# Performance work log

Hardware: AMD Instinct MI355X
Metric: run time of the kernel (lower is better)

Reference implementation:

```python
import jax, jax.numpy as jnp
import numpy as np
from jax import lax

B, T, V, E, H, K = 64, 512, 50257, 300, 128, 3


def setup_inputs() -> dict:
    key = jax.random.key(0)
    ks = jax.random.split(key, 16)
    s = 0.05
    return {
        "tokens": jax.random.randint(ks[0], (B, T), 0, V),
        "emb": jax.random.normal(ks[1], (V, E), jnp.float32) * s,
        # forward LSTM (keras gate order i,f,g,o packed along last axis)
        "Wf": jax.random.normal(ks[2], (E, 4 * H), jnp.float32) * s,
        "Uf": jax.random.normal(ks[3], (H, 4 * H), jnp.float32) * s,
        "bf": jnp.zeros((4 * H,), jnp.float32),
        # backward LSTM
        "Wb": jax.random.normal(ks[4], (E, 4 * H), jnp.float32) * s,
        "Ub": jax.random.normal(ks[5], (H, 4 * H), jnp.float32) * s,
        "bb": jnp.zeros((4 * H,), jnp.float32),
        # dense projection to tagset
        "Wd": jax.random.normal(ks[6], (2 * H, K), jnp.float32) * s,
        "bd": jnp.zeros((K,), jnp.float32),
        # tfa.layers.CRF params: inner kernel, chain transitions, boundaries
        "crf_W": jax.random.normal(ks[7], (K, K), jnp.float32) * s,
        "crf_b": jnp.zeros((K,), jnp.float32),
        "chain": jax.random.normal(ks[8], (K, K), jnp.float32) * s,
        "left_b": jax.random.normal(ks[9], (K,), jnp.float32) * s,
        "right_b": jax.random.normal(ks[10], (K,), jnp.float32) * s,
    }


def _lstm(x, W, U, b):
    """Keras LSTM: gates i,f,g,o; sigmoid recurrent act, tanh cell act."""
    xW = jnp.einsum("btd,dh->bth", x, W) + b  # precompute input GEMM [B,T,4H]
    h0 = jnp.zeros((x.shape[0], U.shape[0]), x.dtype)

    def step(carry, xw):
        h, c = carry
        z = xw + h @ U
        i, f, g, o = jnp.split(z, 4, axis=-1)
        c = jax.nn.sigmoid(f) * c + jax.nn.sigmoid(i) * jnp.tanh(g)
        h = jax.nn.sigmoid(o) * jnp.tanh(c)
        return (h, c), h

    _, hs = lax.scan(step, (h0, h0), jnp.swapaxes(xW, 0, 1))  # [T,B,H]
    return jnp.swapaxes(hs, 0, 1)  # [B,T,H]


def _potentials(tokens, emb, Wf, Uf, bf, Wb, Ub, bb, Wd, bd, crf_W, crf_b, left_b, right_b):
    x = emb[tokens]  # [B,T,E]
    h_fwd = _lstm(x, Wf, Uf, bf)
    h_bwd = _lstm(x[:, ::-1], Wb, Ub, bb)[:, ::-1]
    h = jnp.concatenate([h_fwd, h_bwd], axis=-1)  # [B,T,2H]
    logits = h @ Wd + bd                          # [B,T,K]
    pot = logits @ crf_W + crf_b                  # CRF inner kernel
    pot = pot.at[:, 0].add(left_b).at[:, -1].add(right_b)  # boundary energies
    return pot


def _viterbi(pot, trans):
    """Viterbi decode. pot [B,T,K], trans [K,K] (prev->next)."""
    def step(alpha, p):
        scores = alpha[:, :, None] + trans[None]   # [B,K_prev,K_next]
        bp = jnp.argmax(scores, axis=1)            # [B,K]
        alpha = jnp.max(scores, axis=1) + p
        return alpha, bp

    alpha, bps = lax.scan(step, pot[:, 0], jnp.swapaxes(pot[:, 1:], 0, 1))
    last = jnp.argmax(alpha, axis=-1)  # [B]

    def back(tag, bp):
        prev = jnp.take_along_axis(bp, tag[:, None], axis=1)[:, 0]
        return prev, prev

    _, tags = lax.scan(back, last, bps, reverse=True)  # [T-1,B]
    return jnp.concatenate([jnp.swapaxes(tags, 0, 1), last[:, None]], axis=1)


def reference(tokens, emb, Wf, Uf, bf, Wb, Ub, bb, Wd, bd, crf_W, crf_b, chain, left_b, right_b):
    pot = _potentials(tokens, emb, Wf, Uf, bf, Wb, Ub, bb, Wd, bd, crf_W, crf_b, left_b, right_b)
    decoded = _viterbi(pot, chain)  # [B,T] int
    return decoded, pot
```

## Files before the change

### kernel.cpp

```cpp
#include <hip/hip_runtime.h>
#include <hip/hip_bf16.h>
#include <math.h>

#define BATCH 64
#define TSEQ  512
#define BT    (BATCH*TSEQ)
#define EDIM  300
#define HID   128
#define G4    512
#define KTAG  3

typedef __attribute__((ext_vector_type(8))) short bf16x8;
typedef __attribute__((ext_vector_type(8))) unsigned short u16x8;
typedef __attribute__((ext_vector_type(4))) float f32x4;

__device__ __forceinline__ unsigned short bf16rn(float v) {
    unsigned int u = __float_as_uint(v);
    return (unsigned short)((u + 0x7FFF + ((u >> 16) & 1)) >> 16);
}

__global__ __launch_bounds__(256) void split_kernel(
    const int* __restrict__ tokens, const float* __restrict__ emb,
    const float* __restrict__ Wf, const float* __restrict__ Wb,
    unsigned short* __restrict__ Abf, unsigned short* __restrict__ Bbf)
{
    const int gid = blockIdx.x * 256 + threadIdx.x;
    const int NA = BT * 80;
    if (gid < NA) {
        const int m = gid / 80;
        const int q = gid - m * 80;
        const int kp = q * 8;
        const int seg = kp >= 320;
        const int k0 = kp - (seg ? 320 : 0);
        const float* __restrict__ er = emb + (size_t)tokens[m] * EDIM;
        unsigned short o[8];
        #pragma unroll
        for (int i = 0; i < 8; ++i) {
            const int kk = k0 + i;
            const float v = (kk < EDIM) ? er[kk] : 0.f;
            const unsigned short hi = bf16rn(v);
            o[i] = seg ? bf16rn(v - __uint_as_float((unsigned)hi << 16)) : hi;
        }
        u16x8 w = {o[0], o[1], o[2], o[3], o[4], o[5], o[6], o[7]};
        *(u16x8*)(Abf + (size_t)m * 640 + kp) = w;
    } else {
        const int g2 = gid - NA;
        const int c = g2 / 120;
        const int q = g2 - c * 120;
        const int kp = q * 8;
        const int seg = (kp >= 640) ? 2 : (kp >= 320 ? 1 : 0);
        const int k0 = kp - seg * 320;
        const float* __restrict__ W = (c >= 512) ? Wb : Wf;
        const int cc = c & 511;
        unsigned short o[8];
        #pragma unroll
        for (int i = 0; i < 8; ++i) {
            const int kk = k0 + i;
            const float v = (kk < EDIM) ? W[(size_t)kk * G4 + cc] : 0.f;
            const unsigned short hi = bf16rn(v);
            o[i] = (seg == 2) ? bf16rn(v - __uint_as_float((unsigned)hi << 16)) : hi;
        }
        u16x8 w = {o[0], o[1], o[2], o[3], o[4], o[5], o[6], o[7]};
        *(u16x8*)(Bbf + (size_t)c * 960 + kp) = w;
    }
}

#if defined(__has_builtin)
#if __has_builtin(__builtin_amdgcn_global_load_lds)
#define HAVE_GLL 1
#endif
#endif

__device__ __forceinline__ void gll16(const unsigned short* g, unsigned short* lds_base) {
#ifdef HAVE_GLL
    __builtin_amdgcn_global_load_lds(
        (const __attribute__((address_space(1))) unsigned int*)g,
        (__attribute__((address_space(3))) unsigned int*)lds_base, 16, 0, 0);
#else
    const int l = threadIdx.x & 63;
    *(u16x8*)(lds_base + l * 8) = *(const u16x8*)g;
#endif
}

__global__ __launch_bounds__(256) void gemm_bf16(
    const unsigned short* __restrict__ Abf, const unsigned short* __restrict__ Bbf,
    const float* __restrict__ bf, const float* __restrict__ bb,
    float* __restrict__ xW)
{
    const int n0 = blockIdx.x * 128;
    const int m0 = blockIdx.y * 128;
    const int tid = threadIdx.x;
    const int lane = tid & 63;
    const int wv = tid >> 6;

    const int dir = n0 >> 9;
    const float* __restrict__ bias = dir ? bb : bf;
    const int c0 = n0 & 511;

    __shared__ __align__(16) unsigned short As[128 * 32];
    __shared__ __align__(16) unsigned short Bs[128 * 32];

    f32x4 acc[4][4];
    #pragma unroll
    for (int i = 0; i < 4; ++i)
        #pragma unroll
        for (int j = 0; j < 4; ++j)
            acc[i][j] = (f32x4){0.f, 0.f, 0.f, 0.f};

    const int wm = (wv & 1) * 64;
    const int wn = (wv >> 1) * 64;

    const int r0 = 32 * wv + (lane >> 2);
    const unsigned short* Asrc0 = Abf + (size_t)(m0 + r0)      * 640 + (lane & 3) * 8;
    const unsigned short* Asrc1 = Abf + (size_t)(m0 + r0 + 16) * 640 + (lane & 3) * 8;
    const unsigned short* Bsrc0 = Bbf + (size_t)(n0 + r0)      * 960 + (lane & 3) * 8;
    const unsigned short* Bsrc1 = Bbf + (size_t)(n0 + r0 + 16) * 960 + (lane & 3) * 8;
    unsigned short* Adst0 = &As[(32 * wv)      * 32];
    unsigned short* Adst1 = &As[(32 * wv + 16) * 32];
    unsigned short* Bdst0 = &Bs[(32 * wv)      * 32];
    unsigned short* Bdst1 = &Bs[(32 * wv + 16) * 32];

    for (int s = 0; s < 30; ++s) {
        const int kbA = (s >= 20 ? s - 20 : s) * 32;
        const int kbB = s * 32;
        gll16(Asrc0 + kbA, Adst0);
        gll16(Asrc1 + kbA, Adst1);
        gll16(Bsrc0 + kbB, Bdst0);
        gll16(Bsrc1 + kbB, Bdst1);
        __syncthreads();

        const int kq = (lane >> 4) * 8;
        bf16x8 a[4], b[4];
        #pragma unroll
        for (int f = 0; f < 4; ++f) {
            a[f] = *(const bf16x8*)&As[(wm + f * 16 + (lane & 15)) * 32 + kq];
            b[f] = *(const bf16x8*)&Bs[(wn + f * 16 + (lane & 15)) * 32 + kq];
        }
        #pragma unroll
        for (int fm = 0; fm < 4; ++fm)
            #pragma unroll
            for (int fn = 0; fn < 4; ++fn)
                acc[fm][fn] = __builtin_amdgcn_mfma_f32_16x16x32_bf16(
                    a[fm], b[fn], acc[fm][fn], 0, 0, 0);
        __syncthreads();
    }

    const size_t obase = (size_t)dir * BT * G4;
    #pragma unroll
    for (int fn = 0; fn < 4; ++fn) {
        const int c = c0 + wn + fn * 16 + (lane & 15);
        const float bv = bias[c];
        #pragma unroll
        for (int fm = 0; fm < 4; ++fm) {
            const int mb = m0 + wm + fm * 16 + (lane >> 4) * 4;
            #pragma unroll
            for (int r = 0; r < 4; ++r)
                xW[obase + (size_t)(mb + r) * G4 + c] = acc[fm][fn][r] + bv;
        }
    }
}

__device__ __forceinline__ float fsig(float x) {
    return __builtin_amdgcn_rcpf(1.f + __expf(-x));
}
__device__ __forceinline__ float ftanh(float x) {
    x = fminf(15.f, fmaxf(-15.f, x));
    const float e = __expf(2.f * x);
    return (e - 1.f) * __builtin_amdgcn_rcpf(e + 1.f);
}

#define QXOR1(x) __int_as_float(__builtin_amdgcn_mov_dpp(__float_as_int(x), 0xB1, 0xF, 0xF, true))
#define QXOR2(x) __int_as_float(__builtin_amdgcn_mov_dpp(__float_as_int(x), 0x4E, 0xF, 0xF, true))

#define DECL_G(g) \
  float u##g##_0,u##g##_1,u##g##_2,u##g##_3,u##g##_4,u##g##_5,u##g##_6,u##g##_7, \
        u##g##_8,u##g##_9,u##g##_10,u##g##_11,u##g##_12,u##g##_13,u##g##_14,u##g##_15, \
        u##g##_16,u##g##_17,u##g##_18,u##g##_19,u##g##_20,u##g##_21,u##g##_22,u##g##_23, \
        u##g##_24,u##g##_25,u##g##_26,u##g##_27,u##g##_28,u##g##_29,u##g##_30,u##g##_31;

#define INIT_G(g) { \
  const float* Ug = U + (size_t)(32 * ks) * G4 + g * 128 + j2; \
  u##g##_0 =Ug[ 0*G4]; u##g##_1 =Ug[ 1*G4]; u##g##_2 =Ug[ 2*G4]; u##g##_3 =Ug[ 3*G4]; \
  u##g##_4 =Ug[ 4*G4]; u##g##_5 =Ug[ 5*G4]; u##g##_6 =Ug[ 6*G4]; u##g##_7 =Ug[ 7*G4]; \
  u##g##_8 =Ug[ 8*G4]; u##g##_9 =Ug[ 9*G4]; u##g##_10=Ug[10*G4]; u##g##_11=Ug[11*G4]; \
  u##g##_12=Ug[12*G4]; u##g##_13=Ug[13*G4]; u##g##_14=Ug[14*G4]; u##g##_15=Ug[15*G4]; \
  u##g##_16=Ug[16*G4]; u##g##_17=Ug[17*G4]; u##g##_18=Ug[18*G4]; u##g##_19=Ug[19*G4]; \
  u##g##_20=Ug[20*G4]; u##g##_21=Ug[21*G4]; u##g##_22=Ug[22*G4]; u##g##_23=Ug[23*G4]; \
  u##g##_24=Ug[24*G4]; u##g##_25=Ug[25*G4]; u##g##_26=Ug[26*G4]; u##g##_27=Ug[27*G4]; \
  u##g##_28=Ug[28*G4]; u##g##_29=Ug[29*G4]; u##g##_30=Ug[30*G4]; u##g##_31=Ug[31*G4]; }

#define PIN_G(g) \
  asm volatile("" : "+v"(u##g##_0),"+v"(u##g##_1),"+v"(u##g##_2),"+v"(u##g##_3), \
                    "+v"(u##g##_4),"+v"(u##g##_5),"+v"(u##g##_6),"+v"(u##g##_7), \
                    "+v"(u##g##_8),"+v"(u##g##_9),"+v"(u##g##_10),"+v"(u##g##_11), \
                    "+v"(u##g##_12),"+v"(u##g##_13),"+v"(u##g##_14),"+v"(u##g##_15)); \
  asm volatile("" : "+v"(u##g##_16),"+v"(u##g##_17),"+v"(u##g##_18),"+v"(u##g##_19), \
                    "+v"(u##g##_20),"+v"(u##g##_21),"+v"(u##g##_22),"+v"(u##g##_23), \
                    "+v"(u##g##_24),"+v"(u##g##_25),"+v"(u##g##_26),"+v"(u##g##_27), \
                    "+v"(u##g##_28),"+v"(u##g##_29),"+v"(u##g##_30),"+v"(u##g##_31));

#define MAC4(hv, A, B, C, D) \
  p0 += hv.x*u0_##A + hv.y*u0_##B + hv.z*u0_##C + hv.w*u0_##D; \
  p1 += hv.x*u1_##A + hv.y*u1_##B + hv.z*u1_##C + hv.w*u1_##D; \
  p2 += hv.x*u2_##A + hv.y*u2_##B + hv.z*u2_##C + hv.w*u2_##D; \
  p3 += hv.x*u3_##A + hv.y*u3_##B + hv.z*u3_##C + hv.w*u3_##D;

__global__ __launch_bounds__(512, 2) void lstm_kernel(
    const float* __restrict__ Uf, const float* __restrict__ Ub,
    const float* __restrict__ xW, float* __restrict__ hs)
{
    const int blk = blockIdx.x;
    const int dir = blk >> 6;
    const int tid = threadIdx.x;
    const int j2  = tid >> 2;
    const int ks  = tid & 3;
    const float* __restrict__ U = dir ? Ub : Uf;

    DECL_G(0) DECL_G(1) DECL_G(2) DECL_G(3)
    INIT_G(0) INIT_G(1) INIT_G(2) INIT_G(3)
    PIN_G(0) PIN_G(1) PIN_G(2) PIN_G(3)

    __shared__ __align__(16) float hbuf[2][160];
    if (tid < 128) hbuf[0][tid + (tid >> 5) * 8] = 0.f;
    float c = 0.f;

    const float* __restrict__ xW_blk = xW + (size_t)blk * (TSEQ * G4);
    float* __restrict__ hs_blk = hs + (size_t)blk * (TSEQ * HID);
    __syncthreads();

    int tt = dir ? (TSEQ - 1) : 0;
    const int tstep = dir ? -1 : 1;
    const int xcol = ks * 128 + j2;

    float xw_cur = xW_blk[tt * G4 + xcol];
    float xw_n1  = xW_blk[(tt + tstep) * G4 + xcol];

    for (int t = 0; t < TSEQ; ++t) {
        const int p = t & 1;
        float xw_n2 = 0.f;
        if (t < TSEQ - 2) xw_n2 = xW_blk[(tt + 2 * tstep) * G4 + xcol];

        float p0 = (ks == 0) ? xw_cur : 0.f;
        float p1 = (ks == 1) ? xw_cur : 0.f;
        float p2 = (ks == 2) ? xw_cur : 0.f;
        float p3 = (ks == 3) ? xw_cur : 0.f;

        const float4* hp = (const float4*)&hbuf[p][ks * 40];
        const float4 hA = hp[0], hB = hp[1], hC = hp[2], hD = hp[3];
        const float4 hE = hp[4], hF = hp[5], hG = hp[6], hH = hp[7];
        MAC4(hA, 0, 1, 2, 3)    MAC4(hB, 4, 5, 6, 7)
        MAC4(hC, 8, 9, 10, 11)  MAC4(hD, 12, 13, 14, 15)
        MAC4(hE, 16, 17, 18, 19) MAC4(hF, 20, 21, 22, 23)
        MAC4(hG, 24, 25, 26, 27) MAC4(hH, 28, 29, 30, 31)

        p0 += QXOR1(p0); p1 += QXOR1(p1); p2 += QXOR1(p2); p3 += QXOR1(p3);
        p0 += QXOR2(p0); p1 += QXOR2(p1); p2 += QXOR2(p2); p3 += QXOR2(p3);

        const float ig = fsig(p0);
        const float fg = fsig(p1);
        const float gg = ftanh(p2);
        const float og = fsig(p3);
        c = fg * c + ig * gg;
        const float h = og * ftanh(c);

        if (ks == 0) {
            hbuf[p ^ 1][j2 + (j2 >> 5) * 8] = h;
            hs_blk[tt * HID + j2] = h;
        }
        asm volatile("s_waitcnt lgkmcnt(0)\n\ts_barrier" ::: "memory");
        xw_cur = xw_n1; xw_n1 = xw_n2; tt += tstep;
    }
}

__global__ void prep_kernel(const float* __restrict__ Wd, const float* __restrict__ bd,
                            const float* __restrict__ crf_W, const float* __restrict__ crf_b,
                            float* __restrict__ Wd2, float* __restrict__ b2)
{
    const int u = threadIdx.x;
    #pragma unroll
    for (int k = 0; k < KTAG; ++k) {
        float s = 0.f;
        #pragma unroll
        for (int jj = 0; jj < KTAG; ++jj) s += Wd[u * KTAG + jj] * crf_W[jj * KTAG + k];
        Wd2[u * KTAG + k] = s;
    }
    if (u < KTAG) {
        float s = crf_b[u];
        #pragma unroll
        for (int jj = 0; jj < KTAG; ++jj) s += bd[jj] * crf_W[jj * KTAG + u];
        b2[u] = s;
    }
}

__global__ __launch_bounds__(256) void pot_kernel(
    const float* __restrict__ hs, const float* __restrict__ Wd2,
    const float* __restrict__ b2, const float* __restrict__ left_b,
    const float* __restrict__ right_b, float* __restrict__ pot)
{
    const int wave = blockIdx.x * 4 + (threadIdx.x >> 6);
    const int lane = threadIdx.x & 63;
    const int b = wave >> 9, t = wave & 511;

    const float* __restrict__ hf = hs + ((size_t)b * TSEQ + t) * HID;
    const float* __restrict__ hb = hf + (size_t)BATCH * TSEQ * HID;

    const float x0 = hf[lane], x1 = hf[lane + 64];
    const float x2 = hb[lane], x3 = hb[lane + 64];

    float a[KTAG];
    #pragma unroll
    for (int k = 0; k < KTAG; ++k)
        a[k] = x0 * Wd2[lane * KTAG + k] + x1 * Wd2[(lane + 64) * KTAG + k]
             + x2 * Wd2[(lane + 128) * KTAG + k] + x3 * Wd2[(lane + 192) * KTAG + k];

    #pragma unroll
    for (int off = 32; off; off >>= 1) {
        a[0] += __shfl_xor(a[0], off);
        a[1] += __shfl_xor(a[1], off);
        a[2] += __shfl_xor(a[2], off);
    }

    if (lane < KTAG) {
        float v = a[lane] + b2[lane];
        if (t == 0)        v += left_b[lane];
        if (t == TSEQ - 1) v += right_b[lane];
        pot[(size_t)wave * KTAG + lane] = v;
    }
}

__global__ __launch_bounds__(64) void viterbi_kernel(
    const float* __restrict__ pot, const float* __restrict__ chain,
    float* __restrict__ decoded)
{
    const int b = blockIdx.x;
    const int lane = threadIdx.x;

    __shared__ float p[TSEQ][KTAG];
    __shared__ int bp[TSEQ - 1];
    __shared__ unsigned char tags[TSEQ];

    const float* __restrict__ pb = pot + (size_t)b * TSEQ * KTAG;
    for (int i = lane; i < TSEQ * KTAG; i += 64) ((float*)p)[i] = pb[i];
    __syncthreads();

    if (lane == 0) {
        float tr[KTAG][KTAG];
        #pragma unroll
        for (int i = 0; i < 9; ++i) tr[i / 3][i % 3] = chain[i];

        float a0 = p[0][0], a1 = p[0][1], a2 = p[0][2];
        for (int t = 1; t < TSEQ; ++t) {
            float n[KTAG]; int bpk[KTAG];
            #pragma unroll
            for (int kn = 0; kn < KTAG; ++kn) {
                const float s0 = a0 + tr[0][kn];
                const float s1 = a1 + tr[1][kn];
                const float s2 = a2 + tr[2][kn];
                float best = s0; int arg = 0;
                if (s1 > best) { best = s1; arg = 1; }
                if (s2 > best) { best = s2; arg = 2; }
                n[kn] = best + p[t][kn];
                bpk[kn] = arg;
            }
            bp[t - 1] = bpk[0] | (bpk[1] << 2) | (bpk[2] << 4);
            a0 = n[0]; a1 = n[1]; a2 = n[2];
        }
        int tag = 0; float best = a0;
        if (a1 > best) { best = a1; tag = 1; }
        if (a2 > best) { best = a2; tag = 2; }
        tags[TSEQ - 1] = (unsigned char)tag;
        for (int t = TSEQ - 2; t >= 0; --t) {
            tag = (bp[t] >> (2 * tag)) & 3;
            tags[t] = (unsigned char)tag;
        }
    }
    __syncthreads();
    for (int t = lane; t < TSEQ; t += 64)
        decoded[(size_t)b * TSEQ + t] = (float)tags[t];
}

extern "C" void kernel_launch(void* const* d_in, const int* in_sizes, int n_in,
                              void* d_out, int out_size, void* d_ws, size_t ws_size,
                              hipStream_t stream) {
    const int*   tokens  = (const int*)d_in[0];
    const float* emb     = (const float*)d_in[1];
    const float* Wf      = (const float*)d_in[2];
    const float* Uf      = (const float*)d_in[3];
    const float* bf      = (const float*)d_in[4];
    const float* Wb      = (const float*)d_in[5];
    const float* Ub      = (const float*)d_in[6];
    const float* bb      = (const float*)d_in[7];
    const float* Wd      = (const float*)d_in[8];
    const float* bd      = (const float*)d_in[9];
    const float* crf_W   = (const float*)d_in[10];
    const float* crf_b   = (const float*)d_in[11];
    const float* chain   = (const float*)d_in[12];
    const float* left_b  = (const float*)d_in[13];
    const float* right_b = (const float*)d_in[14];

    float* out = (float*)d_out;
    float* pot = out + BT;

    float* xW  = (float*)d_ws;
    unsigned short* Abf = (unsigned short*)(xW + (size_t)2 * BT * G4);
    unsigned short* Bbf = Abf + (size_t)BT * 640;
    float* hs  = (float*)Abf;
    float* Wd2 = (float*)(Bbf + (size_t)1024 * 960);
    float* b2  = Wd2 + 2 * HID * KTAG;

    const int nsplit = (BT * 80 + 1024 * 120) / 256;
    split_kernel<<<nsplit, 256, 0, stream>>>(tokens, emb, Wf, Wb, Abf, Bbf);
    prep_kernel<<<1, 256, 0, stream>>>(Wd, bd, crf_W, crf_b, Wd2, b2);
    dim3 gG(8, BT / 128);
    gemm_bf16<<<gG, 256, 0, stream>>>(Abf, Bbf, bf, bb, xW);
    lstm_kernel<<<128, 512, 0, stream>>>(Uf, Ub, xW, hs);
    pot_kernel<<<BT / 4, 256, 0, stream>>>(hs, Wd2, b2, left_b, right_b, pot);
    viterbi_kernel<<<BATCH, 64, 0, stream>>>(pot, chain, out);
}
```

Before: 593.2 us.

## Double-buffer GEMM LDS tiles and prefetch Viterbi potentials one step ahead

The bf16 input-projection GEMM now keeps two LDS buffers, so the global-to-LDS load for the next k-step is issued before the MFMAs on the current step, and one barrier per iteration is removed. Separately, the serial Viterbi forward loop loads the next timestep's potentials from shared memory one iteration early, taking LDS latency off the dependency chain. The cost is doubled LDS use in the GEMM, which may lower occupancy. The Viterbi change only helps if the loop was bound by LDS latency and not by the max/compare chain.

```diff
diff --git a/kernel.cpp b/kernel.cpp
--- a/kernel.cpp
+++ b/kernel.cpp
@@ -97,8 +97,8 @@
     const float* __restrict__ bias = dir ? bb : bf;
     const int c0 = n0 & 511;
 
-    __shared__ __align__(16) unsigned short As[128 * 32];
-    __shared__ __align__(16) unsigned short Bs[128 * 32];
+    __shared__ __align__(16) unsigned short As[2][128 * 32];
+    __shared__ __align__(16) unsigned short Bs[2][128 * 32];
 
     f32x4 acc[4][4];
     #pragma unroll
@@ -115,26 +115,29 @@
     const unsigned short* Asrc1 = Abf + (size_t)(m0 + r0 + 16) * 640 + (lane & 3) * 8;
     const unsigned short* Bsrc0 = Bbf + (size_t)(n0 + r0)      * 960 + (lane & 3) * 8;
     const unsigned short* Bsrc1 = Bbf + (size_t)(n0 + r0 + 16) * 960 + (lane & 3) * 8;
-    unsigned short* Adst0 = &As[(32 * wv)      * 32];
-    unsigned short* Adst1 = &As[(32 * wv + 16) * 32];
-    unsigned short* Bdst0 = &Bs[(32 * wv)      * 32];
-    unsigned short* Bdst1 = &Bs[(32 * wv + 16) * 32];
-
+    const int d0 = (32 * wv) * 32, d1 = (32 * wv + 16) * 32;
+
+#define STAGE(buf, s) { \
+    const int kbA_ = ((s) >= 20 ? (s) - 20 : (s)) * 32; \
+    const int kbB_ = (s) * 32; \
+    gll16(Asrc0 + kbA_, &As[buf][d0]); \
+    gll16(Asrc1 + kbA_, &As[buf][d1]); \
+    gll16(Bsrc0 + kbB_, &Bs[buf][d0]); \
+    gll16(Bsrc1 + kbB_, &Bs[buf][d1]); }
+
+    STAGE(0, 0)
+    __syncthreads();
+
+    int cur = 0;
     for (int s = 0; s < 30; ++s) {
-        const int kbA = (s >= 20 ? s - 20 : s) * 32;
-        const int kbB = s * 32;
-        gll16(Asrc0 + kbA, Adst0);
-        gll16(Asrc1 + kbA, Adst1);
-        gll16(Bsrc0 + kbB, Bdst0);
-        gll16(Bsrc1 + kbB, Bdst1);
-        __syncthreads();
+        if (s < 29) STAGE(cur ^ 1, s + 1)
 
         const int kq = (lane >> 4) * 8;
         bf16x8 a[4], b[4];
         #pragma unroll
         for (int f = 0; f < 4; ++f) {
-            a[f] = *(const bf16x8*)&As[(wm + f * 16 + (lane & 15)) * 32 + kq];
-            b[f] = *(const bf16x8*)&Bs[(wn + f * 16 + (lane & 15)) * 32 + kq];
+            a[f] = *(const bf16x8*)&As[cur][(wm + f * 16 + (lane & 15)) * 32 + kq];
+            b[f] = *(const bf16x8*)&Bs[cur][(wn + f * 16 + (lane & 15)) * 32 + kq];
         }
         #pragma unroll
         for (int fm = 0; fm < 4; ++fm)
@@ -142,8 +145,11 @@
             for (int fn = 0; fn < 4; ++fn)
                 acc[fm][fn] = __builtin_amdgcn_mfma_f32_16x16x32_bf16(
                     a[fm], b[fn], acc[fm][fn], 0, 0, 0);
+
         __syncthreads();
-    }
+        cur ^= 1;
+    }
+#undef STAGE
 
     const size_t obase = (size_t)dir * BT * G4;
     #pragma unroll
@@ -349,8 +355,14 @@
         for (int i = 0; i < 9; ++i) tr[i / 3][i % 3] = chain[i];
 
         float a0 = p[0][0], a1 = p[0][1], a2 = p[0][2];
+        float q0 = p[1][0], q1 = p[1][1], q2 = p[1][2];
         for (int t = 1; t < TSEQ; ++t) {
+            const float pt0 = q0, pt1 = q1, pt2 = q2;
+            if (t + 1 < TSEQ) {
+                q0 = p[t + 1][0]; q1 = p[t + 1][1]; q2 = p[t + 1][2];
+            }
             float n[KTAG]; int bpk[KTAG];
+            const float ptv[KTAG] = {pt0, pt1, pt2};
             #pragma unroll
             for (int kn = 0; kn < KTAG; ++kn) {
                 const float s0 = a0 + tr[0][kn];
@@ -359,7 +371,7 @@
                 float best = s0; int arg = 0;
                 if (s1 > best) { best = s1; arg = 1; }
                 if (s2 > best) { best = s2; arg = 2; }
-                n[kn] = best + p[t][kn];
+                n[kn] = best + ptv[kn];
                 bpk[kn] = arg;
             }
             bp[t - 1] = bpk[0] | (bpk[1] << 2) | (bpk[2] << 4);
```

New measurement: 589.5 us. Within noise of the previous version (-0.6%).
